# Kernel optimization log

Hardware: AMD Instinct MI355X
Metric: run time of the kernel (lower is better)

## Reference

```python
import jax, jax.numpy as jnp
from jax import lax
import numpy as np

VOCAB, EMB, HID, NLAYERS, NCLS = 32000, 512, 1024, 2, 32000
B, T = 64, 256


def setup_inputs() -> dict:
    key = jax.random.key(0)
    ks = jax.random.split(key, 12)
    s_in = 1.0 / np.sqrt(HID)
    inp = {
        "tokens": jax.random.randint(ks[0], (B, T), 0, VOCAB),
        "emb": jax.random.normal(ks[1], (VOCAB, EMB), jnp.float32),
        "W_ih0": jax.random.uniform(ks[2], (4 * HID, EMB), jnp.float32, -s_in, s_in),
        "W_hh0": jax.random.uniform(ks[3], (4 * HID, HID), jnp.float32, -s_in, s_in),
        "b_ih0": jax.random.uniform(ks[4], (4 * HID,), jnp.float32, -s_in, s_in),
        "b_hh0": jax.random.uniform(ks[5], (4 * HID,), jnp.float32, -s_in, s_in),
        "W_ih1": jax.random.uniform(ks[6], (4 * HID, HID), jnp.float32, -s_in, s_in),
        "W_hh1": jax.random.uniform(ks[7], (4 * HID, HID), jnp.float32, -s_in, s_in),
        "b_ih1": jax.random.uniform(ks[8], (4 * HID,), jnp.float32, -s_in, s_in),
        "b_hh1": jax.random.uniform(ks[9], (4 * HID,), jnp.float32, -s_in, s_in),
        "fc_w": jax.random.uniform(ks[10], (NCLS, HID), jnp.float32, -s_in, s_in),
        "fc_b": jax.random.uniform(ks[11], (NCLS,), jnp.float32, -s_in, s_in),
    }
    return inp


def _lstm_layer(x, W_ih, W_hh, b_ih, b_hh):
    # x: [B, T, in]; PyTorch gate order i, f, g, o
    Bb = x.shape[0]
    H = W_hh.shape[1]
    # precompute input-to-hidden contribution for all timesteps (one big GEMM)
    xg = jnp.einsum('bti,gi->btg', x, W_ih) + b_ih + b_hh  # [B, T, 4H]

    def step(carry, xg_t):
        h, c = carry
        g = xg_t + h @ W_hh.T  # [B, 4H]
        i, f, gg, o = jnp.split(g, 4, axis=-1)
        i = jax.nn.sigmoid(i)
        f = jax.nn.sigmoid(f)
        gg = jnp.tanh(gg)
        o = jax.nn.sigmoid(o)
        c = f * c + i * gg
        h = o * jnp.tanh(c)
        return (h, c), h

    h0 = jnp.zeros((Bb, H), x.dtype)
    (_, _), hs = lax.scan(step, (h0, h0), jnp.swapaxes(xg, 0, 1))  # hs: [T, B, H]
    return jnp.swapaxes(hs, 0, 1)


def reference(tokens, emb, W_ih0, W_hh0, b_ih0, b_hh0, W_ih1, W_hh1, b_ih1, b_hh1, fc_w, fc_b):
    x = emb[tokens]  # [B, T, EMB]
    x = _lstm_layer(x, W_ih0, W_hh0, b_ih0, b_hh0)
    x = _lstm_layer(x, W_ih1, W_hh1, b_ih1, b_hh1)
    return x[:, -1, :] @ fc_w.T + fc_b  # [B, NCLS]
```

## Files before the change

kernel.cpp:

```cpp
#include <hip/hip_runtime.h>
#include <hip/hip_bf16.h>

#define B_ 64
#define T_ 256
#define EMB_ 512
#define HID_ 1024
#define G4_ 4096
#define NCLS_ 32000
#define BH (B_ * HID_)

typedef _Float16 f16;
typedef _Float16 f16x8 __attribute__((ext_vector_type(8)));
typedef _Float16 f16x4 __attribute__((ext_vector_type(4)));
typedef _Float16 f16x2 __attribute__((ext_vector_type(2)));
typedef float f32x4 __attribute__((ext_vector_type(4)));
typedef unsigned long long u64;

__device__ __forceinline__ float sigm(float x) { return 1.f / (1.f + __expf(-x)); }

__device__ __forceinline__ void stg_u32(unsigned* p, unsigned v) {
  __hip_atomic_store(p, v, __ATOMIC_RELAXED, __HIP_MEMORY_SCOPE_AGENT);
}
__device__ __forceinline__ void stg_u64(u64* p, u64 v) {
  __hip_atomic_store(p, v, __ATOMIC_RELAXED, __HIP_MEMORY_SCOPE_AGENT);
}
__device__ __forceinline__ unsigned ldg_u32(const unsigned* p) {
  return __hip_atomic_load(p, __ATOMIC_RELAXED, __HIP_MEMORY_SCOPE_AGENT);
}
__device__ __forceinline__ void fadd_u32(unsigned* p) {
  __hip_atomic_fetch_add(p, 1u, __ATOMIC_RELAXED, __HIP_MEMORY_SCOPE_AGENT);
}


__global__ __launch_bounds__(256) void cvt_kernel(const float* __restrict__ src,
                                                  f16* __restrict__ dst, int n4) {
  int i = blockIdx.x * 256 + threadIdx.x;
  if (i < n4) {
    float4 v = ((const float4*)src)[i];
    f16x4 o = {(f16)v.x, (f16)v.y, (f16)v.z, (f16)v.w};
    *(f16x4*)(dst + (size_t)i * 4) = o;
  }
}

__global__ __launch_bounds__(256) void bsum_kernel(const float* __restrict__ a0,
                                                   const float* __restrict__ b0,
                                                   float* __restrict__ o0,
                                                   const float* __restrict__ a1,
                                                   const float* __restrict__ b1,
                                                   float* __restrict__ o1) {
  int i = blockIdx.x * 256 + threadIdx.x;
  if (i < G4_) {
    o0[i] = a0[i] + b0[i];
    o1[i] = a1[i] + b1[i];
  }
}

__global__ __launch_bounds__(128) void gather_kernel(const int* __restrict__ tokens,
                                                     const float* __restrict__ emb,
                                                     f16* __restrict__ x0) {
  int blk = blockIdx.x;
  int t = blk >> 6, b = blk & 63;
  int tok = tokens[b * T_ + t];
  float4 v = ((const float4*)(emb + (size_t)tok * EMB_))[threadIdx.x];
  f16x4 o = {(f16)v.x, (f16)v.y, (f16)v.z, (f16)v.w};
  *(f16x4*)(x0 + (size_t)blk * EMB_ + threadIdx.x * 4) = o;
}

#define KPH(AP, ASTR, WCOL0, ACOL0, N)                                          \
  _Pragma("unroll") for (int f = 0; f < (N); ++f) {                             \
    const f16* ap0 = (AP) + (size_t)r0 * (ASTR) + ((ACOL0) + f) * 32 + lk * 8;  \
    const f16* ap1 = (AP) + (size_t)r1 * (ASTR) + ((ACOL0) + f) * 32 + lk * 8;  \
    f16x8 a0 = *(const f16x8*)ap0;                                              \
    f16x8 a1 = *(const f16x8*)ap1;                                              \
    f16x8 b0 = *(const f16x8*)(wr0 + ((WCOL0) + f) * 32);                       \
    f16x8 b1 = *(const f16x8*)(wr1 + ((WCOL0) + f) * 32);                       \
    acc00 = __builtin_amdgcn_mfma_f32_16x16x32_f16(a0, b0, acc00, 0, 0, 0);     \
    acc01 = __builtin_amdgcn_mfma_f32_16x16x32_f16(a0, b1, acc01, 0, 0, 0);     \
    acc10 = __builtin_amdgcn_mfma_f32_16x16x32_f16(a1, b0, acc10, 0, 0, 0);     \
    acc11 = __builtin_amdgcn_mfma_f32_16x16x32_f16(a1, b1, acc11, 0, 0, 0);     \
  }

#define KPHB(AP, WCOL0, AG0, N)                                                 \
  _Pragma("unroll") for (int f = 0; f < (N); ++f) {                             \
    const f16* ap0 = (AP) + (((AG0) + f) * 4 + lk) * 512 + r0 * 8;              \
    const f16* ap1 = (AP) + (((AG0) + f) * 4 + lk) * 512 + r1 * 8;              \
    f16x8 a0 = *(const f16x8*)ap0;                                              \
    f16x8 a1 = *(const f16x8*)ap1;                                              \
    f16x8 b0 = *(const f16x8*)(wr0 + ((WCOL0) + f) * 32);                       \
    f16x8 b1 = *(const f16x8*)(wr1 + ((WCOL0) + f) * 32);                       \
    acc00 = __builtin_amdgcn_mfma_f32_16x16x32_f16(a0, b0, acc00, 0, 0, 0);     \
    acc01 = __builtin_amdgcn_mfma_f32_16x16x32_f16(a0, b1, acc01, 0, 0, 0);     \
    acc10 = __builtin_amdgcn_mfma_f32_16x16x32_f16(a1, b0, acc10, 0, 0, 0);     \
    acc11 = __builtin_amdgcn_mfma_f32_16x16x32_f16(a1, b1, acc11, 0, 0, 0);     \
  }

__global__ __launch_bounds__(512, 2) void persist_kernel(
    const f16* __restrict__ x0, const f16* __restrict__ w0i,
    const f16* __restrict__ w0h, const f16* __restrict__ w1i,
    const f16* __restrict__ w1h, const float* __restrict__ b0s,
    const float* __restrict__ b1s, f16* __restrict__ h0r,
    f16* __restrict__ h1r, unsigned* flags) {
  __shared__ f16 Ws[32 * 2056];
  __shared__ float red[6 * 64 * 17];
  __shared__ float cst[512];

  const int layer = blockIdx.x >> 7;
  const int slice = blockIdx.x & 127;
  const int tid = threadIdx.x;
  const int lane = tid & 63, wave = tid >> 6;
  const int mi = wave >> 2, kq = wave & 3;
  const int lr = lane & 15, lk = lane >> 4;
  const int j0 = slice * 8;

  const f16* whh = layer ? w1h : w0h;
  const f16* wih = layer ? w1i : w0i;
  const float* bs = layer ? b1s : b0s;
  f16* hown = layer ? h1r : h0r;
  const int KI = layer ? HID_ : EMB_;
  const int nch = (HID_ + KI) >> 3;
  const int wstr = HID_ + KI + 8;

  unsigned* ctr_own = flags + (layer ? 256 : 0);
  unsigned* ctr_l0 = flags;

  for (int r = wave * 4; r < wave * 4 + 4; ++r) {
    int grow = (r >> 3) * HID_ + j0 + (r & 7);
    for (int c = lane; c < nch; c += 64) {
      int kk = c * 8;
      const f16* src = (kk < HID_) ? (whh + (size_t)grow * HID_ + kk)
                                   : (wih + (size_t)grow * KI + (kk - HID_));
      *(uint4*)(Ws + r * wstr + kk) = *(const uint4*)src;
    }
  }
  float brg[4][4];
  {
    int u4 = (tid & 1) * 4;
#pragma unroll
    for (int g = 0; g < 4; ++g)
#pragma unroll
      for (int e = 0; e < 4; ++e) brg[g][e] = bs[g * HID_ + j0 + u4 + e];
  }
  for (int i = tid; i < 512; i += 512) cst[i] = 0.f;
  __syncthreads();

  const int r0 = mi * 32 + lr, r1 = r0 + 16;
  const f16* wr0 = Ws + lr * wstr + lk * 8;
  const f16* wr1 = wr0 + 16 * wstr;

#define WAITC(CBASE, TGT)                                                   \
  {                                                                         \
    if (wave == 0) {                                                        \
      const unsigned tg_ = (TGT);                                           \
      unsigned v_ = tg_;                                                    \
      if (lane < 8) v_ = ldg_u32((CBASE) + lane * 32);                      \
      int iters_ = 0;                                                       \
      while (!__all((int)(v_ >= tg_))) {                                    \
        if (++iters_ > 4000000) break;                    \
        __builtin_amdgcn_s_sleep(2);                                        \
        if (lane < 8) v_ = ldg_u32((CBASE) + lane * 32);                    \
      }                                                                     \
    }                                                                       \
    __syncthreads();                                                        \
  }

  for (int s = 0; s < T_; ++s) {
    f32x4 acc00 = {}, acc01 = {}, acc10 = {}, acc11 = {};

    if (layer == 0) {
      const f16* xb = x0 + (size_t)s * (B_ * EMB_);
      KPH(xb, EMB_, 32 + kq * 4, kq * 4, 4)
      WAITC(ctr_own, (unsigned)(16 * s))
      const f16* hb = h0r + (size_t)s * BH;
      KPHB(hb, kq * 8, kq * 8, 8)
    } else {
      WAITC(ctr_l0, (unsigned)(16 * (s + 1)))
      const f16* xb = h0r + (size_t)(s + 1) * BH;
      KPHB(xb, 32 + kq * 8, kq * 8, 8)
      WAITC(ctr_own, (unsigned)(16 * s))
      const f16* hb = h1r + (size_t)s * BH;
      KPHB(hb, kq * 8, kq * 8, 8)
    }

    if (kq) {
      float* rp = red + ((mi * 3 + kq - 1) * 64 + lane) * 17;
      *(f32x4*)(rp) = acc00;      *(f32x4*)(rp + 4) = acc01;
      *(f32x4*)(rp + 8) = acc10;  *(f32x4*)(rp + 12) = acc11;
    }
    __syncthreads();
    if (!kq) {
#pragma unroll
      for (int q = 0; q < 3; ++q) {
        const float* rp = red + ((mi * 3 + q) * 64 + lane) * 17;
        acc00 += *(const f32x4*)(rp);      acc01 += *(const f32x4*)(rp + 4);
        acc10 += *(const f32x4*)(rp + 8);  acc11 += *(const f32x4*)(rp + 12);
      }
    }
    __syncthreads();
    if (!kq) {
      float* pre = red;
      int col = mi * 32 + lk * 4;
      *(f32x4*)(pre + (0 + lr) * 68 + col) = acc00;
      *(f32x4*)(pre + (16 + lr) * 68 + col) = acc01;
      *(f32x4*)(pre + (0 + lr) * 68 + col + 16) = acc10;
      *(f32x4*)(pre + (16 + lr) * 68 + col + 16) = acc11;
    }
    __syncthreads();

    if (tid < 128) {
      const float* pre = red;
      f16* hout = hown + (size_t)(s + 1) * BH;
      int b = tid >> 1, u4 = (tid & 1) * 4;
      f16x4 hv;
#pragma unroll
      for (int e = 0; e < 4; ++e) {
        int r = u4 + e;
        float pi = pre[(0 * 8 + r) * 68 + b] + brg[0][e];
        float pf = pre[(1 * 8 + r) * 68 + b] + brg[1][e];
        float pg = pre[(2 * 8 + r) * 68 + b] + brg[2][e];
        float po = pre[(3 * 8 + r) * 68 + b] + brg[3][e];
        float ig = sigm(pi), fg = sigm(pf), gg = tanhf(pg), og = sigm(po);
        float cn = fg * cst[b * 8 + r] + ig * gg;
        cst[b * 8 + r] = cn;
        hv[e] = (f16)(og * tanhf(cn));
      }
      stg_u64((u64*)(hout + slice * 512 + b * 8 + u4),
              __builtin_bit_cast(u64, hv));
    }

    asm volatile("s_waitcnt vmcnt(0)" ::: "memory");
    __syncthreads();
    if (tid == 0) fadd_u32(&ctr_own[(blockIdx.x & 7) * 32]);
  }
}

__global__ __launch_bounds__(256) void fc_kernel(const f16* __restrict__ A,
                                                 const float* __restrict__ fcw,
                                                 const float* __restrict__ fcb,
                                                 float* __restrict__ out) {
  const int n0 = blockIdx.x * 64;
  __shared__ char smem[18432];
  f16* As = (f16*)smem;
  f16* Bs = (f16*)(smem + 9216);
  const int tid = threadIdx.x;
  const int lane = tid & 63, wave = tid >> 6;
  const int wm = wave & 1, wn = wave >> 1;
  const int lr = lane & 15, lk = lane >> 4;
  f32x4 acc[2][2] = {};

  for (int kt = 0; kt < HID_ / 64; ++kt) {
    const int k0 = kt * 64;
    __syncthreads();
#pragma unroll
    for (int i = 0; i < 2; ++i) {
      int id = tid + 256 * i;
      int r = id >> 3, c8 = id & 7;
      uint4 av = *(const uint4*)(A + (size_t)((k0 >> 3) + c8) * 512 + r * 8);
      *(uint4*)(As + r * 72 + c8 * 8) = av;
    }
#pragma unroll
    for (int i = 0; i < 4; ++i) {
      int id = tid + 256 * i;
      int r = id >> 4, c4 = id & 15;
      float4 v = *(const float4*)(fcw + (size_t)(n0 + r) * HID_ + k0 + c4 * 4);
      f16x4 o = {(f16)v.x, (f16)v.y, (f16)v.z, (f16)v.w};
      *(f16x4*)(Bs + r * 72 + c4 * 4) = o;
    }
    __syncthreads();
#pragma unroll
    for (int ks = 0; ks < 2; ++ks) {
      f16x8 a0 = *(const f16x8*)(As + (wm * 32 + lr) * 72 + ks * 32 + lk * 8);
      f16x8 a1 = *(const f16x8*)(As + (wm * 32 + 16 + lr) * 72 + ks * 32 + lk * 8);
      f16x8 b0 = *(const f16x8*)(Bs + (wn * 32 + lr) * 72 + ks * 32 + lk * 8);
      f16x8 b1 = *(const f16x8*)(Bs + (wn * 32 + 16 + lr) * 72 + ks * 32 + lk * 8);
      acc[0][0] = __builtin_amdgcn_mfma_f32_16x16x32_f16(a0, b0, acc[0][0], 0, 0, 0);
      acc[0][1] = __builtin_amdgcn_mfma_f32_16x16x32_f16(a0, b1, acc[0][1], 0, 0, 0);
      acc[1][0] = __builtin_amdgcn_mfma_f32_16x16x32_f16(a1, b0, acc[1][0], 0, 0, 0);
      acc[1][1] = __builtin_amdgcn_mfma_f32_16x16x32_f16(a1, b1, acc[1][1], 0, 0, 0);
    }
  }

#pragma unroll
  for (int mf = 0; mf < 2; ++mf)
#pragma unroll
    for (int nf = 0; nf < 2; ++nf) {
      int n = n0 + wn * 32 + nf * 16 + lr;
      float bias = fcb[n];
      int bbase = wm * 32 + mf * 16 + lk * 4;
#pragma unroll
      for (int rg = 0; rg < 4; ++rg)
        out[(size_t)(bbase + rg) * NCLS_ + n] = acc[mf][nf][rg] + bias;
    }
}


extern "C" void kernel_launch(void* const* d_in, const int* in_sizes, int n_in,
                              void* d_out, int out_size, void* d_ws,
                              size_t ws_size, hipStream_t stream) {
  const int* tokens = (const int*)d_in[0];
  const float* emb = (const float*)d_in[1];
  const float* W_ih0 = (const float*)d_in[2];
  const float* W_hh0 = (const float*)d_in[3];
  const float* b_ih0 = (const float*)d_in[4];
  const float* b_hh0 = (const float*)d_in[5];
  const float* W_ih1 = (const float*)d_in[6];
  const float* W_hh1 = (const float*)d_in[7];
  const float* b_ih1 = (const float*)d_in[8];
  const float* b_hh1 = (const float*)d_in[9];
  const float* fc_w = (const float*)d_in[10];
  const float* fc_b = (const float*)d_in[11];
  float* out = (float*)d_out;

  char* ws = (char*)d_ws;
  size_t off = 0;
  auto carve = [&](size_t bytes) -> char* {
    char* p = ws + off;
    off += (bytes + 255) & ~(size_t)255;
    return p;
  };
  f16* w0i = (f16*)carve((size_t)G4_ * EMB_ * 2);
  f16* w0h = (f16*)carve((size_t)G4_ * HID_ * 2);
  f16* w1i = (f16*)carve((size_t)G4_ * HID_ * 2);
  f16* w1h = (f16*)carve((size_t)G4_ * HID_ * 2);
  f16* x0 = (f16*)carve((size_t)T_ * B_ * EMB_ * 2);
  float* b0s = (float*)carve(G4_ * 4);
  float* b1s = (float*)carve(G4_ * 4);
  f16* h0r = (f16*)carve(257ull * BH * 2);
  f16* h1r = (f16*)carve(257ull * BH * 2);
  unsigned* flags = (unsigned*)carve(1024 * 4);

  hipMemsetAsync(flags, 0, 1024 * 4, stream);
  hipMemsetAsync(h0r, 0, (size_t)BH * 2, stream);
  hipMemsetAsync(h1r, 0, (size_t)BH * 2, stream);

  cvt_kernel<<<(G4_ * EMB_ / 4 + 255) / 256, 256, 0, stream>>>(W_ih0, w0i, G4_ * EMB_ / 4);
  cvt_kernel<<<(G4_ * HID_ / 4 + 255) / 256, 256, 0, stream>>>(W_hh0, w0h, G4_ * HID_ / 4);
  cvt_kernel<<<(G4_ * HID_ / 4 + 255) / 256, 256, 0, stream>>>(W_ih1, w1i, G4_ * HID_ / 4);
  cvt_kernel<<<(G4_ * HID_ / 4 + 255) / 256, 256, 0, stream>>>(W_hh1, w1h, G4_ * HID_ / 4);
  bsum_kernel<<<(G4_ + 255) / 256, 256, 0, stream>>>(b_ih0, b_hh0, b0s, b_ih1, b_hh1, b1s);
  gather_kernel<<<T_ * B_, 128, 0, stream>>>(tokens, emb, x0);

  persist_kernel<<<256, 512, 0, stream>>>(x0, w0i, w0h, w1i, w1h, b0s, b1s,
                                          h0r, h1r, flags);

  fc_kernel<<<NCLS_ / 64, 256, 0, stream>>>(h1r + 256ull * BH, fc_w, fc_b, out);
}
```

Measured before the change: 2.015 ms.

## Use aggregator block to republish step counters to replicated epoch flags

Rather than every block polling eight sharded arrival counters, one aggregator block per layer polls them and writes a per-step epoch to eight replicated flags. The other blocks each spin on a single replicated flag. This cuts the number of polling loads per step and spreads them across copies, with the aim of lowering barrier contention and latency. The cost is an extra hop through the aggregator, which is now on the critical path, and the aggregator also sleeps for shorter intervals while polling.

```diff
diff --git a/kernel.cpp b/kernel.cpp
--- a/kernel.cpp
+++ b/kernel.cpp
@@ -94,6 +94,38 @@
     acc11 = __builtin_amdgcn_mfma_f32_16x16x32_f16(a1, b1, acc11, 0, 0, 0);     \
   }
 
+#define AGG_WAIT_PUB(CBASE, RBASE, CTGT, EPOCH)                             \
+  {                                                                         \
+    if (wave == 0) {                                                        \
+      const unsigned tg_ = (CTGT);                                          \
+      unsigned v_ = tg_;                                                    \
+      if (lane < 8) v_ = ldg_u32((CBASE) + lane * 32);                      \
+      int iters_ = 0;                                                       \
+      while (!__all((int)(v_ >= tg_))) {                                    \
+        if (++iters_ > 4000000) break;                    \
+        __builtin_amdgcn_s_sleep(1);                                        \
+        if (lane < 8) v_ = ldg_u32((CBASE) + lane * 32);                    \
+      }                                                                     \
+      if (lane < 8) stg_u32((RBASE) + lane * 64, (EPOCH));                  \
+    }                                                                       \
+    __syncthreads();                                                        \
+  }
+
+#define REPL_WAIT(RADDR, TGT)                                               \
+  {                                                                         \
+    if (wave == 0) {                                                        \
+      const unsigned tg_ = (TGT);                                           \
+      unsigned v_ = ldg_u32(RADDR);                                         \
+      int iters_ = 0;                                                       \
+      while (v_ < tg_) {                                                    \
+        if (++iters_ > 4000000) break;                    \
+        __builtin_amdgcn_s_sleep(2);                                        \
+        v_ = ldg_u32(RADDR);                                                \
+      }                                                                     \
+    }                                                                       \
+    __syncthreads();                                                        \
+  }
+
 __global__ __launch_bounds__(512, 2) void persist_kernel(
     const f16* __restrict__ x0, const f16* __restrict__ w0i,
     const f16* __restrict__ w0h, const f16* __restrict__ w1i,
@@ -111,6 +143,7 @@
   const int mi = wave >> 2, kq = wave & 3;
   const int lr = lane & 15, lk = lane >> 4;
   const int j0 = slice * 8;
+  const bool isagg = (slice == 0);
 
   const f16* whh = layer ? w1h : w0h;
   const f16* wih = layer ? w1i : w0i;
@@ -121,7 +154,10 @@
   const int wstr = HID_ + KI + 8;
 
   unsigned* ctr_own = flags + (layer ? 256 : 0);
-  unsigned* ctr_l0 = flags;
+  unsigned* repl_own = flags + (layer ? 1536 : 1024);
+  unsigned* repl_l0 = flags + 1024;
+  unsigned* my_repl_own = repl_own + (blockIdx.x & 7) * 64;
+  unsigned* my_repl_l0 = repl_l0 + (blockIdx.x & 7) * 64;
 
   for (int r = wave * 4; r < wave * 4 + 4; ++r) {
     int grow = (r >> 3) * HID_ + j0 + (r & 7);
@@ -147,36 +183,22 @@
   const f16* wr0 = Ws + lr * wstr + lk * 8;
   const f16* wr1 = wr0 + 16 * wstr;
 
-#define WAITC(CBASE, TGT)                                                   \
-  {                                                                         \
-    if (wave == 0) {                                                        \
-      const unsigned tg_ = (TGT);                                           \
-      unsigned v_ = tg_;                                                    \
-      if (lane < 8) v_ = ldg_u32((CBASE) + lane * 32);                      \
-      int iters_ = 0;                                                       \
-      while (!__all((int)(v_ >= tg_))) {                                    \
-        if (++iters_ > 4000000) break;                    \
-        __builtin_amdgcn_s_sleep(2);                                        \
-        if (lane < 8) v_ = ldg_u32((CBASE) + lane * 32);                    \
-      }                                                                     \
-    }                                                                       \
-    __syncthreads();                                                        \
-  }
-
   for (int s = 0; s < T_; ++s) {
     f32x4 acc00 = {}, acc01 = {}, acc10 = {}, acc11 = {};
 
     if (layer == 0) {
       const f16* xb = x0 + (size_t)s * (B_ * EMB_);
       KPH(xb, EMB_, 32 + kq * 4, kq * 4, 4)
-      WAITC(ctr_own, (unsigned)(16 * s))
+      if (isagg) { AGG_WAIT_PUB(ctr_own, repl_own, (unsigned)(16 * s), (unsigned)s) }
+      else       { REPL_WAIT(my_repl_own, (unsigned)s) }
       const f16* hb = h0r + (size_t)s * BH;
       KPHB(hb, kq * 8, kq * 8, 8)
     } else {
-      WAITC(ctr_l0, (unsigned)(16 * (s + 1)))
+      REPL_WAIT(my_repl_l0, (unsigned)(s + 1))
       const f16* xb = h0r + (size_t)(s + 1) * BH;
       KPHB(xb, 32 + kq * 8, kq * 8, 8)
-      WAITC(ctr_own, (unsigned)(16 * s))
+      if (isagg) { AGG_WAIT_PUB(ctr_own, repl_own, (unsigned)(16 * s), (unsigned)s) }
+      else       { REPL_WAIT(my_repl_own, (unsigned)s) }
       const f16* hb = h1r + (size_t)s * BH;
       KPHB(hb, kq * 8, kq * 8, 8)
     }
@@ -230,6 +252,19 @@
     asm volatile("s_waitcnt vmcnt(0)" ::: "memory");
     __syncthreads();
     if (tid == 0) fadd_u32(&ctr_own[(blockIdx.x & 7) * 32]);
+  }
+
+  if (layer == 0 && isagg && wave == 0) {
+    const unsigned tg = (unsigned)(16 * T_);
+    unsigned v = tg;
+    if (lane < 8) v = ldg_u32(ctr_own + lane * 32);
+    int iters = 0;
+    while (!__all((int)(v >= tg))) {
+      if (++iters > 4000000) break;
+      __builtin_amdgcn_s_sleep(1);
+      if (lane < 8) v = ldg_u32(ctr_own + lane * 32);
+    }
+    if (lane < 8) stg_u32(repl_own + lane * 64, (unsigned)T_);
   }
 }
 
@@ -326,9 +361,9 @@
   float* b1s = (float*)carve(G4_ * 4);
   f16* h0r = (f16*)carve(257ull * BH * 2);
   f16* h1r = (f16*)carve(257ull * BH * 2);
-  unsigned* flags = (unsigned*)carve(1024 * 4);
-
-  hipMemsetAsync(flags, 0, 1024 * 4, stream);
+  unsigned* flags = (unsigned*)carve(2048 * 4);
+
+  hipMemsetAsync(flags, 0, 2048 * 4, stream);
   hipMemsetAsync(h0r, 0, (size_t)BH * 2, stream);
   hipMemsetAsync(h1r, 0, (size_t)BH * 2, stream);
 
```

Result: no change. 2.014 ms (-0.0%).

## Replace block-wide step barrier with per-sector counters waited on per wave

Applied to the files above, without the earlier changes.

Each block now bumps a counter for its own sector, a group of 16 slices that write one contiguous k-range of h, instead of a round-robin counter. Each wave polls only the sector counters that cover its k-chunks and starts MFMA work on a chunk as soon as that sector is done, with no block-wide __syncthreads wait. This lets computation overlap with other blocks that are still finishing, but every wave now spins on atomics, which adds polling traffic.

```diff
diff --git a/kernel.cpp b/kernel.cpp
--- a/kernel.cpp
+++ b/kernel.cpp
@@ -12,15 +12,11 @@
 typedef _Float16 f16;
 typedef _Float16 f16x8 __attribute__((ext_vector_type(8)));
 typedef _Float16 f16x4 __attribute__((ext_vector_type(4)));
-typedef _Float16 f16x2 __attribute__((ext_vector_type(2)));
 typedef float f32x4 __attribute__((ext_vector_type(4)));
 typedef unsigned long long u64;
 
 __device__ __forceinline__ float sigm(float x) { return 1.f / (1.f + __expf(-x)); }
 
-__device__ __forceinline__ void stg_u32(unsigned* p, unsigned v) {
-  __hip_atomic_store(p, v, __ATOMIC_RELAXED, __HIP_MEMORY_SCOPE_AGENT);
-}
 __device__ __forceinline__ void stg_u64(u64* p, u64 v) {
   __hip_atomic_store(p, v, __ATOMIC_RELAXED, __HIP_MEMORY_SCOPE_AGENT);
 }
@@ -94,6 +90,18 @@
     acc11 = __builtin_amdgcn_mfma_f32_16x16x32_f16(a1, b1, acc11, 0, 0, 0);     \
   }
 
+#define WAITS(ADDR, TGT)                                                    \
+  {                                                                         \
+    const unsigned tg_ = (TGT);                                             \
+    unsigned v_ = ldg_u32(ADDR);                                            \
+    int it_ = 0;                                                            \
+    while (v_ < tg_) {                                                      \
+      if (++it_ > 4000000) break;    \
+      __builtin_amdgcn_s_sleep(2);                                          \
+      v_ = ldg_u32(ADDR);                                                   \
+    }                                                                       \
+  }
+
 __global__ __launch_bounds__(512, 2) void persist_kernel(
     const f16* __restrict__ x0, const f16* __restrict__ w0i,
     const f16* __restrict__ w0h, const f16* __restrict__ w1i,
@@ -106,6 +114,7 @@
 
   const int layer = blockIdx.x >> 7;
   const int slice = blockIdx.x & 127;
+  const int sector = slice >> 4;
   const int tid = threadIdx.x;
   const int lane = tid & 63, wave = tid >> 6;
   const int mi = wave >> 2, kq = wave & 3;
@@ -147,38 +156,34 @@
   const f16* wr0 = Ws + lr * wstr + lk * 8;
   const f16* wr1 = wr0 + 16 * wstr;
 
-#define WAITC(CBASE, TGT)                                                   \
-  {                                                                         \
-    if (wave == 0) {                                                        \
-      const unsigned tg_ = (TGT);                                           \
-      unsigned v_ = tg_;                                                    \
-      if (lane < 8) v_ = ldg_u32((CBASE) + lane * 32);                      \
-      int iters_ = 0;                                                       \
-      while (!__all((int)(v_ >= tg_))) {                                    \
-        if (++iters_ > 4000000) break;                    \
-        __builtin_amdgcn_s_sleep(2);                                        \
-        if (lane < 8) v_ = ldg_u32((CBASE) + lane * 32);                    \
-      }                                                                     \
-    }                                                                       \
-    __syncthreads();                                                        \
-  }
-
   for (int s = 0; s < T_; ++s) {
     f32x4 acc00 = {}, acc01 = {}, acc10 = {}, acc11 = {};
 
     if (layer == 0) {
       const f16* xb = x0 + (size_t)s * (B_ * EMB_);
       KPH(xb, EMB_, 32 + kq * 4, kq * 4, 4)
-      WAITC(ctr_own, (unsigned)(16 * s))
       const f16* hb = h0r + (size_t)s * BH;
-      KPHB(hb, kq * 8, kq * 8, 8)
+#pragma unroll
+      for (int sq = 0; sq < 2; ++sq) {
+        int sec = kq * 2 + sq;
+        WAITS(ctr_own + sec * 32, 16u * (unsigned)s)
+        KPHB(hb, sec * 4, sec * 4, 4)
+      }
     } else {
-      WAITC(ctr_l0, (unsigned)(16 * (s + 1)))
       const f16* xb = h0r + (size_t)(s + 1) * BH;
-      KPHB(xb, 32 + kq * 8, kq * 8, 8)
-      WAITC(ctr_own, (unsigned)(16 * s))
+#pragma unroll
+      for (int sq = 0; sq < 2; ++sq) {
+        int sec = kq * 2 + sq;
+        WAITS(ctr_l0 + sec * 32, 16u * (unsigned)(s + 1))
+        KPHB(xb, 32 + sec * 4, sec * 4, 4)
+      }
       const f16* hb = h1r + (size_t)s * BH;
-      KPHB(hb, kq * 8, kq * 8, 8)
+#pragma unroll
+      for (int sq = 0; sq < 2; ++sq) {
+        int sec = kq * 2 + sq;
+        WAITS(ctr_own + sec * 32, 16u * (unsigned)s)
+        KPHB(hb, sec * 4, sec * 4, 4)
+      }
     }
 
     if (kq) {
@@ -229,7 +234,7 @@
 
     asm volatile("s_waitcnt vmcnt(0)" ::: "memory");
     __syncthreads();
-    if (tid == 0) fadd_u32(&ctr_own[(blockIdx.x & 7) * 32]);
+    if (tid == 0) fadd_u32(&ctr_own[sector * 32]);
   }
 }
 
```

Result: faster. 1.831 ms (median of 2 runs) (-9.1%).
